# Kernel tuning notes

Hardware: AMD Instinct MI355X
Metric: run time of the kernel (lower is better)

The kernel has to match this reference:

```python
import jax, jax.numpy as jnp
import numpy as np

H = 128  # LSTM hidden size


def lstm_layer(x, Wih, Whh, bih, bhh):
    # x: [B, T, Fin]; Wih: [4H, Fin]; Whh: [4H, H]; biases: [4H]
    xg = jnp.einsum('btf,gf->btg', x, Wih) + bih  # precompute input gates [B,T,4H]
    B = x.shape[0]
    h0 = jnp.zeros((B, H), x.dtype)
    c0 = jnp.zeros((B, H), x.dtype)

    def step(carry, xt):
        h, c = carry
        g = xt + h @ Whh.T + bhh  # [B,4H]
        i, f, gg, o = jnp.split(g, 4, axis=-1)  # torch gate order: i,f,g,o
        i = jax.nn.sigmoid(i)
        f = jax.nn.sigmoid(f)
        gg = jnp.tanh(gg)
        o = jax.nn.sigmoid(o)
        c = f * c + i * gg
        h = o * jnp.tanh(c)
        return (h, c), h

    (hT, cT), hs = jax.lax.scan(step, (h0, c0), jnp.swapaxes(xg, 0, 1))
    return jnp.swapaxes(hs, 0, 1), hT  # all-step outputs [B,T,H], final h [B,H]


def setup_inputs() -> dict:
    key = jax.random.key(0)
    ks = jax.random.split(key, 20)
    B, T, F = 512, 912, 32
    s = 1.0 / np.sqrt(H)  # torch LSTM/Linear init scale
    u = lambda k, shape: jax.random.uniform(k, shape, jnp.float32, -s, s)
    return {
        'x': jax.random.normal(ks[0], (B, T, F), jnp.float32),
        'Wih0': u(ks[1], (4 * H, F)),
        'Whh0': u(ks[2], (4 * H, H)),
        'bih0': u(ks[3], (4 * H,)),
        'bhh0': u(ks[4], (4 * H,)),
        'Wih123': u(ks[5], (3, 4 * H, H)),
        'Whh123': u(ks[6], (3, 4 * H, H)),
        'bih123': u(ks[7], (3, 4 * H)),
        'bhh123': u(ks[8], (3, 4 * H)),
        'Wopt': u(ks[9], (4, H)), 'bopt': u(ks[10], (4,)),
        'Wlot': u(ks[11], (4, H)), 'blot': u(ks[12], (4,)),
        'Wtp': u(ks[13], (4, H)), 'btp': u(ks[14], (4,)),
        'Wsl': u(ks[15], (4, H)), 'bsl': u(ks[16], (4,)),
    }


def reference(x, Wih0, Whh0, bih0, bhh0, Wih123, Whh123, bih123, bhh123,
              Wopt, bopt, Wlot, blot, Wtp, btp, Wsl, bsl):
    out, h0f = lstm_layer(x, Wih0, Whh0, bih0, bhh0)
    finals = [h0f]
    for l in range(3):  # fixed small layer loop
        out, hf = lstm_layer(out, Wih123[l], Whh123[l], bih123[l], bhh123[l])
        finals.append(hf)
    hN = jnp.stack(finals)  # h_n: [4, B, H] (final hidden per layer, as torch returns)
    # heads: Sequential applies softmax/sigmoid once, forward applies it again
    opt = jax.nn.softmax(jax.nn.softmax(hN @ Wopt.T + bopt, axis=-1), axis=-1)
    lot = jax.nn.sigmoid(jax.nn.sigmoid(hN @ Wlot.T + blot))
    tp = jax.nn.sigmoid(jax.nn.sigmoid(hN @ Wtp.T + btp))
    sl = jax.nn.sigmoid(jax.nn.sigmoid(hN @ Wsl.T + bsl))
    return (opt, tp, sl, lot)
```

## Files before the change

kernel.cpp:

```cpp
#include <hip/hip_runtime.h>

#define DEV __device__ __forceinline__

typedef __attribute__((ext_vector_type(8))) short short8;
typedef __attribute__((ext_vector_type(4))) float floatx4;
typedef unsigned long long ull;

static constexpr int B_ = 512, T_ = 912, H_ = 128, F_ = 32;
static constexpr size_t HN_OFF   = 1024;
static constexpr size_t XT_OFF   = HN_OFF + (size_t)4 * 512 * 128 * 2;
static constexpr size_t RING_OFF = XT_OFF + (size_t)T_ * B_ * F_ * 2;
static constexpr size_t RING_BPG = 8 * 32768;

template <int N> struct IC { static constexpr int value = N; };

DEV unsigned short bf16rne(float f) {
    unsigned u = __builtin_bit_cast(unsigned, f);
    u += 0x7FFFu + ((u >> 16) & 1u);
    return (unsigned short)(u >> 16);
}
DEV float bf16tof(unsigned short u) {
    return __builtin_bit_cast(float, ((unsigned)u) << 16);
}
DEV float fastsig(float y) {
    return __builtin_amdgcn_rcpf(1.f + __builtin_amdgcn_exp2f(y));
}
DEV float sigm(float x) { return fastsig(-1.44269504f * x); }
DEV unsigned ald(const unsigned* p) {
    return __hip_atomic_load(p, __ATOMIC_RELAXED, __HIP_MEMORY_SCOPE_AGENT);
}
DEV void ast32(unsigned* p, unsigned v) {
    __hip_atomic_store(p, v, __ATOMIC_RELAXED, __HIP_MEMORY_SCOPE_AGENT);
}
DEV ull ald8(const ull* p) {
    return __hip_atomic_load(p, __ATOMIC_RELAXED, __HIP_MEMORY_SCOPE_AGENT);
}
DEV void ast8(ull* p, ull v) {
    __hip_atomic_store(p, v, __ATOMIC_RELAXED, __HIP_MEMORY_SCOPE_AGENT);
}
DEV void bar_fast() {
    asm volatile("s_waitcnt lgkmcnt(0)\n\ts_barrier" ::: "memory");
}

__global__ __launch_bounds__(256) void xpose(const float* __restrict__ x,
                                             unsigned short* __restrict__ xT) {
    int tid = blockIdx.x * 256 + threadIdx.x;
    if (tid >= B_ * T_ * 4) return;
    int k = tid & 3;
    int r = tid >> 2;
    int b = r / T_;
    int t = r - b * T_;
    const float* p = x + ((size_t)r * 32 + k * 8);
    short8 v;
#pragma unroll
    for (int j = 0; j < 8; j++) v[j] = (short)bf16rne(p[j]);
    *(short8*)(xT + ((size_t)t * 512 + b) * 32 + k * 8) = v;
}

__global__ __launch_bounds__(512, 2) void lstm_scan(
    const float* __restrict__ Wih0, const float* __restrict__ Whh0,
    const float* __restrict__ bih0, const float* __restrict__ bhh0,
    const float* __restrict__ Wih123, const float* __restrict__ Whh123,
    const float* __restrict__ bih123, const float* __restrict__ bhh123,
    char* __restrict__ ws) {
    const int tid  = threadIdx.x;
    const int wv   = tid >> 6;
    const int lane = tid & 63;
    const int col  = lane & 15;
    const int quad = lane >> 4;
    const int layer = blockIdx.x >> 5;
    const int grp   = blockIdx.x & 31;
    const int b0    = grp * 16;

    unsigned* flags = (unsigned*)ws;
    unsigned* cons  = (unsigned*)(ws + 512);
    char* hN8 = ws + HN_OFF;
    const char* xTB = ws + XT_OFF;

    __shared__ unsigned short Ah[16][16][132];
    __shared__ unsigned short Xl[16][16][132];
    char* AhB = (char*)Ah;
    char* XlB = (char*)Xl;

    for (int i = tid; i < 16 * 16 * 132; i += 512) {
        ((unsigned short*)Ah)[i] = 0;
        ((unsigned short*)Xl)[i] = 0;
    }

    short8 wh[4][4];
    short8 wx[4][4];
    float  bias_q[4];
    {
        const float *Wih, *Whh, *bih, *bhh;
        int kin, KX;
        if (layer == 0) { Wih = Wih0; Whh = Whh0; bih = bih0; bhh = bhh0; kin = 32; KX = 1; }
        else {
            Wih = Wih123 + (size_t)(layer - 1) * 512 * 128;
            Whh = Whh123 + (size_t)(layer - 1) * 512 * 128;
            bih = bih123 + (size_t)(layer - 1) * 512;
            bhh = bhh123 + (size_t)(layer - 1) * 512;
            kin = 128; KX = 4;
        }
#pragma unroll
        for (int q = 0; q < 4; q++) {
            const float sc = (q == 2) ? -2.88539008f : -1.44269504f;
            int row = q * 128 + wv * 16 + col;
            bias_q[q] = (bih[row] + bhh[row]) * sc;
#pragma unroll
            for (int kt = 0; kt < 4; kt++) {
                const float* ph = Whh + (size_t)row * 128 + kt * 32 + quad * 8;
                short8 v;
#pragma unroll
                for (int j = 0; j < 8; j++) v[j] = (short)bf16rne(ph[j] * sc);
                wh[q][kt] = v;
            }
#pragma unroll
            for (int kt = 0; kt < 4; kt++) {
                short8 v = {0, 0, 0, 0, 0, 0, 0, 0};
                if (kt < KX) {
                    const float* px = Wih + (size_t)row * kin + kt * 32 + quad * 8;
#pragma unroll
                    for (int j = 0; j < 8; j++) v[j] = (short)bf16rne(px[j] * sc);
                }
                wx[q][kt] = v;
            }
        }
    }

    unsigned* myflag   = &flags[layer * 32 + grp];
    unsigned* prevflag = &flags[(layer > 0 ? layer - 1 : 0) * 32 + grp];
    unsigned* mycons   = &cons[(layer > 0 ? layer - 1 : 0) * 32 + grp];
    unsigned* nextcons = &cons[layer * 32 + grp];
    char* prodRing = ws + RING_OFF + (size_t)(layer * 32 + grp) * RING_BPG;
    char* consRing = ws + RING_OFF + (size_t)((layer > 0 ? layer - 1 : 0) * 32 + grp) * RING_BPG;

    const int ahrd  = col * 264 + quad * 16;
    const int hwr   = (quad * 4) * 264 + (wv * 16 + col) * 2;
    const int exOff = (tid >> 5) * 264 + (tid & 31) * 8;
    const int consOff = (tid >> 5) * 256 + (tid & 31) * 8;
    const int xgOff = (tid >> 6) * 32768 + b0 * 64 + (tid & 63) * 16;
    const int xlw0  = (tid >> 6) * 4224 + ((tid >> 2) & 15) * 264 + (tid & 3) * 16;

    ull    xin[8];
    short8 xv = {0, 0, 0, 0, 0, 0, 0, 0};
    unsigned pf = 0, pc = 0;
    float c4[4] = {0.f, 0.f, 0.f, 0.f};
    floatx4 accx[4];

    __syncthreads();

    if (layer > 0) {
        if (tid == 0) { while (ald(prevflag) < 2u) {} }
        __syncthreads();
#pragma unroll
        for (int j = 0; j < 16; j++) {
            ull d = ald8((const ull*)(consRing + (size_t)j * 4096 + consOff));
            *(ull*)(XlB + exOff + j * 4224) = d;
        }
    } else {
#pragma unroll
        for (int c0 = 0; c0 < 2; c0++) {
            short8 v = *(const short8*)(xTB + (size_t)c0 * 262144 + xgOff);
            *(short8*)(XlB + xlw0 + c0 * 33792) = v;
        }
    }
    __syncthreads();

    {
        short8 ax0[4];
#pragma unroll
        for (int kt = 0; kt < 4; kt++)
            ax0[kt] = *(const short8*)(XlB + ahrd + 0 * 4224 + kt * 64);
#pragma unroll
        for (int q = 0; q < 4; q++) {
            floatx4 a = {bias_q[q], bias_q[q], bias_q[q], bias_q[q]};
            accx[q] = a;
        }
#pragma unroll
        for (int kt = 0; kt < 4; kt++)
#pragma unroll
            for (int q = 0; q < 4; q++)
                accx[q] = __builtin_amdgcn_mfma_f32_16x16x32_bf16(ax0[kt], wx[q][kt], accx[q], 0, 0, 0);
    }

    int c = 0;
    auto step = [&](auto UC) {
        constexpr int u   = UC.value;
        constexpr bool bnd = (u == 0 || u == 8);
        constexpr bool stg = (u == 3 || u == 11);
        constexpr bool ver = (u == 7 || u == 15);
        constexpr int sph = (u < 8) ? 8 : 0;
        const int cc = c + (u >> 3);
        if (bnd) {
            if (tid == 0) {
                if (layer > 0 && cc <= 111) pf = ald(prevflag);
                if (layer < 3 && cc >= 8)   pc = ald(nextcons);
            }
            if (layer < 3 && cc >= 1) {
                char* rb = prodRing + (size_t)((cc - 1) & 7) * 32768 + tid * 8;
#pragma unroll
                for (int p = 0; p < 8; p++) {
                    ull hv = *(const ull*)(AhB + exOff + (sph + p) * 4224);
                    ast8((ull*)(rb + p * 4096), hv);
                }
            }
            if (layer > 0 && cc <= 112) {
                const char* rb2 = consRing + (size_t)((cc + 1) & 7) * 32768 + consOff;
#pragma unroll
                for (int j = 0; j < 8; j++)
                    xin[j] = ald8((const ull*)(rb2 + j * 4096));
            }
            if (layer == 0 && cc <= 112)
                xv = *(const short8*)(xTB + (size_t)(cc + 1) * 262144 + xgOff);
        }
        if (stg) {
            if (layer > 0) {
#pragma unroll
                for (int j = 0; j < 8; j++)
                    *(ull*)(XlB + exOff + (sph + j) * 4224) = xin[j];
            } else {
                *(short8*)(XlB + xlw0 + sph * 4224) = xv;
            }
        }
        short8 ah[4], axn[4];
#pragma unroll
        for (int kt = 0; kt < 4; kt++) {
            ah[kt]  = *(const short8*)(AhB + ahrd + ((u + 15) & 15) * 4224 + kt * 64);
            axn[kt] = *(const short8*)(XlB + ahrd + ((u + 1) & 15) * 4224 + kt * 64);
        }
        floatx4 acc[4];
#pragma unroll
        for (int q = 0; q < 4; q++) acc[q] = accx[q];
#pragma unroll
        for (int kt = 0; kt < 4; kt++)
#pragma unroll
            for (int q = 0; q < 4; q++)
                acc[q] = __builtin_amdgcn_mfma_f32_16x16x32_bf16(ah[kt], wh[q][kt], acc[q], 0, 0, 0);
#pragma unroll
        for (int q = 0; q < 4; q++) {
            floatx4 a = {bias_q[q], bias_q[q], bias_q[q], bias_q[q]};
            accx[q] = a;
        }
#pragma unroll
        for (int r = 0; r < 4; r++) {
            float iv = fastsig(acc[0][r]);
            float fv = fastsig(acc[1][r]);
            float gr = fastsig(acc[2][r]);
            float ov = fastsig(acc[3][r]);
#pragma unroll
            for (int q = 0; q < 4; q++)
                accx[q] = __builtin_amdgcn_mfma_f32_16x16x32_bf16(axn[r], wx[q][r], accx[q], 0, 0, 0);
            float gt = 2.f * gr - 1.f;
            float cv = fv * c4[r] + iv * gt;
            c4[r] = cv;
            float rc = fastsig(-2.88539008f * cv);
            float hv = ov * (2.f * rc - 1.f);
            *(unsigned short*)(AhB + hwr + u * 4224 + r * 264) = bf16rne(hv);
        }
        if (stg) {
            __syncthreads();
            if (tid == 0) {
                if (layer < 3 && cc >= 1) ast32(myflag, (unsigned)cc);
                if (layer > 0) ast32(mycons, (unsigned)(cc + 2));
            }
        } else {
            if (ver && tid == 0) {
                if (layer > 0 && cc <= 111) {
                    unsigned tgt = cc + 3;
                    if (pf < tgt) while (ald(prevflag) < tgt) {}
                }
                if (layer < 3 && cc >= 8) {
                    unsigned tgt = cc - 7;
                    if (pc < tgt) while (ald(nextcons) < tgt) {}
                }
            }
            bar_fast();
        }
    };

    for (c = 0; c < 114; c += 2) {
        step(IC<0>{});  step(IC<1>{});  step(IC<2>{});  step(IC<3>{});
        step(IC<4>{});  step(IC<5>{});  step(IC<6>{});  step(IC<7>{});
        step(IC<8>{});  step(IC<9>{});  step(IC<10>{}); step(IC<11>{});
        step(IC<12>{}); step(IC<13>{}); step(IC<14>{}); step(IC<15>{});
    }

    if (layer < 3) {
        char* rb = prodRing + (size_t)(113 & 7) * 32768 + tid * 8;
#pragma unroll
        for (int p = 0; p < 8; p++) {
            ull hv = *(const ull*)(AhB + exOff + (8 + p) * 4224);
            ast8((ull*)(rb + p * 4096), hv);
        }
    }
    __syncthreads();
    if (tid == 0 && layer < 3) ast32(myflag, 114u);
    {
        ull hv = *(const ull*)(AhB + exOff + 15 * 4224);
        *(ull*)(hN8 + ((size_t)layer * 512 + b0 + (tid >> 5)) * 256 + (tid & 31) * 8) = hv;
    }
}

__global__ __launch_bounds__(256) void heads(
    const unsigned short* __restrict__ hN,
    const float* __restrict__ Wopt, const float* __restrict__ bopt,
    const float* __restrict__ Wlot, const float* __restrict__ blot,
    const float* __restrict__ Wtp,  const float* __restrict__ btp,
    const float* __restrict__ Wsl,  const float* __restrict__ bsl,
    float* __restrict__ out) {
    int tid = blockIdx.x * 256 + threadIdx.x;
    if (tid >= 4 * 4 * 512) return;
    int b  = tid & 511;
    int l  = (tid >> 9) & 3;
    int hd = tid >> 11;
    const float *W, *bb;
    if      (hd == 0) { W = Wopt; bb = bopt; }
    else if (hd == 1) { W = Wtp;  bb = btp;  }
    else if (hd == 2) { W = Wsl;  bb = bsl;  }
    else              { W = Wlot; bb = blot; }
    const unsigned short* h = hN + ((size_t)l * 512 + b) * 128;
    float z0 = bb[0], z1 = bb[1], z2 = bb[2], z3 = bb[3];
    for (int i = 0; i < 128; i++) {
        float hv = bf16tof(h[i]);
        z0 += hv * W[0 * 128 + i];
        z1 += hv * W[1 * 128 + i];
        z2 += hv * W[2 * 128 + i];
        z3 += hv * W[3 * 128 + i];
    }
    float o0, o1, o2, o3;
    if (hd == 0) {
        float m = fmaxf(fmaxf(z0, z1), fmaxf(z2, z3));
        float e0 = __builtin_amdgcn_exp2f((z0 - m) * 1.44269504f);
        float e1 = __builtin_amdgcn_exp2f((z1 - m) * 1.44269504f);
        float e2 = __builtin_amdgcn_exp2f((z2 - m) * 1.44269504f);
        float e3 = __builtin_amdgcn_exp2f((z3 - m) * 1.44269504f);
        float rs = __builtin_amdgcn_rcpf(e0 + e1 + e2 + e3);
        float p0 = e0 * rs, p1 = e1 * rs, p2 = e2 * rs, p3 = e3 * rs;
        float m2 = fmaxf(fmaxf(p0, p1), fmaxf(p2, p3));
        float f0 = __builtin_amdgcn_exp2f((p0 - m2) * 1.44269504f);
        float f1 = __builtin_amdgcn_exp2f((p1 - m2) * 1.44269504f);
        float f2 = __builtin_amdgcn_exp2f((p2 - m2) * 1.44269504f);
        float f3 = __builtin_amdgcn_exp2f((p3 - m2) * 1.44269504f);
        float rs2 = __builtin_amdgcn_rcpf(f0 + f1 + f2 + f3);
        o0 = f0 * rs2; o1 = f1 * rs2; o2 = f2 * rs2; o3 = f3 * rs2;
    } else {
        o0 = sigm(sigm(z0)); o1 = sigm(sigm(z1));
        o2 = sigm(sigm(z2)); o3 = sigm(sigm(z3));
    }
    float* o = out + (size_t)hd * 8192 + ((size_t)l * 512 + b) * 4;
    o[0] = o0; o[1] = o1; o[2] = o2; o[3] = o3;
}

extern "C" void kernel_launch(void* const* d_in, const int* in_sizes, int n_in,
                              void* d_out, int out_size, void* d_ws, size_t ws_size,
                              hipStream_t stream) {
    (void)in_sizes; (void)n_in; (void)out_size; (void)ws_size;
    const float* x      = (const float*)d_in[0];
    const float* Wih0   = (const float*)d_in[1];
    const float* Whh0   = (const float*)d_in[2];
    const float* bih0   = (const float*)d_in[3];
    const float* bhh0   = (const float*)d_in[4];
    const float* Wih123 = (const float*)d_in[5];
    const float* Whh123 = (const float*)d_in[6];
    const float* bih123 = (const float*)d_in[7];
    const float* bhh123 = (const float*)d_in[8];
    const float* Wopt = (const float*)d_in[9];
    const float* bopt = (const float*)d_in[10];
    const float* Wlot = (const float*)d_in[11];
    const float* blot = (const float*)d_in[12];
    const float* Wtp  = (const float*)d_in[13];
    const float* btp  = (const float*)d_in[14];
    const float* Wsl  = (const float*)d_in[15];
    const float* bsl  = (const float*)d_in[16];
    char* ws = (char*)d_ws;

    hipMemsetAsync(ws, 0, 1024, stream);
    xpose<<<(B_ * T_ * 4 + 255) / 256, 256, 0, stream>>>(x, (unsigned short*)(ws + XT_OFF));
    lstm_scan<<<128, 512, 0, stream>>>(Wih0, Whh0, bih0, bhh0,
                                       Wih123, Whh123, bih123, bhh123, ws);
    heads<<<32, 256, 0, stream>>>((const unsigned short*)(ws + HN_OFF),
                                  Wopt, bopt, Wlot, blot, Wtp, btp, Wsl, bsl,
                                  (float*)d_out);
}
```

Baseline: 2.123 ms.

## Load layer inputs directly into MFMA registers and shrink LDS staging ring

Removes the LDS staging buffer for layer inputs. Each step now loads its x operand fragments straight from the global ring, or from the transposed input for layer 0, into double-buffered registers one step ahead. The per-step input projection is fused back into the same step instead of overlapping with the previous step's activations. The h history buffer shrinks from 16 to 8 slots, and producer stores move from chunked bursts to one per step. It also adds s_setprio around the MFMA block. This is meant to cut LDS traffic and footprint, at the cost of putting the x-projection MFMAs on the serial critical path and changing the flag protocol arithmetic.

```diff
diff --git a/kernel.cpp b/kernel.cpp
--- a/kernel.cpp
+++ b/kernel.cpp
@@ -5,6 +5,7 @@
 typedef __attribute__((ext_vector_type(8))) short short8;
 typedef __attribute__((ext_vector_type(4))) float floatx4;
 typedef unsigned long long ull;
+typedef __attribute__((ext_vector_type(2))) unsigned long long ull2;
 
 static constexpr int B_ = 512, T_ = 912, H_ = 128, F_ = 32;
 static constexpr size_t HN_OFF   = 1024;
@@ -71,21 +72,17 @@
     const int layer = blockIdx.x >> 5;
     const int grp   = blockIdx.x & 31;
     const int b0    = grp * 16;
+    const bool lay0 = (layer == 0);
 
     unsigned* flags = (unsigned*)ws;
     unsigned* cons  = (unsigned*)(ws + 512);
     char* hN8 = ws + HN_OFF;
     const char* xTB = ws + XT_OFF;
 
-    __shared__ unsigned short Ah[16][16][132];
-    __shared__ unsigned short Xl[16][16][132];
+    __shared__ unsigned short Ah[8][16][132];
     char* AhB = (char*)Ah;
-    char* XlB = (char*)Xl;
-
-    for (int i = tid; i < 16 * 16 * 132; i += 512) {
-        ((unsigned short*)Ah)[i] = 0;
-        ((unsigned short*)Xl)[i] = 0;
-    }
+
+    for (int i = tid; i < 8 * 16 * 132; i += 512) ((unsigned short*)Ah)[i] = 0;
 
     short8 wh[4][4];
     short8 wx[4][4];
@@ -137,140 +134,136 @@
     const int ahrd  = col * 264 + quad * 16;
     const int hwr   = (quad * 4) * 264 + (wv * 16 + col) * 2;
     const int exOff = (tid >> 5) * 264 + (tid & 31) * 8;
-    const int consOff = (tid >> 5) * 256 + (tid & 31) * 8;
-    const int xgOff = (tid >> 6) * 32768 + b0 * 64 + (tid & 63) * 16;
-    const int xlw0  = (tid >> 6) * 4224 + ((tid >> 2) & 15) * 264 + (tid & 3) * 16;
-
-    ull    xin[8];
-    short8 xv = {0, 0, 0, 0, 0, 0, 0, 0};
+    const int xro   = col * 256 + quad * 16;
+    const int xoffA = (b0 + col) * 64 + quad * 16;
+
+    ull     xnA[8], xnB[8];
+    short8  ax0A = {0,0,0,0,0,0,0,0}, ax0B = ax0A;
     unsigned pf = 0, pc = 0;
     float c4[4] = {0.f, 0.f, 0.f, 0.f};
-    floatx4 accx[4];
 
     __syncthreads();
 
-    if (layer > 0) {
+    if (!lay0) {
         if (tid == 0) { while (ald(prevflag) < 2u) {} }
         __syncthreads();
-#pragma unroll
-        for (int j = 0; j < 16; j++) {
-            ull d = ald8((const ull*)(consRing + (size_t)j * 4096 + consOff));
-            *(ull*)(XlB + exOff + j * 4224) = d;
+        const char* rp = consRing + xro;
+#pragma unroll
+        for (int kt = 0; kt < 4; kt++) {
+            xnA[2 * kt]     = ald8((const ull*)(rp + kt * 64));
+            xnA[2 * kt + 1] = ald8((const ull*)(rp + kt * 64 + 8));
         }
     } else {
-#pragma unroll
-        for (int c0 = 0; c0 < 2; c0++) {
-            short8 v = *(const short8*)(xTB + (size_t)c0 * 262144 + xgOff);
-            *(short8*)(XlB + xlw0 + c0 * 33792) = v;
-        }
-    }
-    __syncthreads();
-
-    {
-        short8 ax0[4];
-#pragma unroll
-        for (int kt = 0; kt < 4; kt++)
-            ax0[kt] = *(const short8*)(XlB + ahrd + 0 * 4224 + kt * 64);
-#pragma unroll
-        for (int q = 0; q < 4; q++) {
-            floatx4 a = {bias_q[q], bias_q[q], bias_q[q], bias_q[q]};
-            accx[q] = a;
-        }
-#pragma unroll
-        for (int kt = 0; kt < 4; kt++)
-#pragma unroll
-            for (int q = 0; q < 4; q++)
-                accx[q] = __builtin_amdgcn_mfma_f32_16x16x32_bf16(ax0[kt], wx[q][kt], accx[q], 0, 0, 0);
+        ax0A = *(const short8*)(xTB + xoffA);
     }
 
     int c = 0;
     auto step = [&](auto UC) {
         constexpr int u   = UC.value;
-        constexpr bool bnd = (u == 0 || u == 8);
-        constexpr bool stg = (u == 3 || u == 11);
-        constexpr bool ver = (u == 7 || u == 15);
-        constexpr int sph = (u < 8) ? 8 : 0;
-        const int cc = c + (u >> 3);
-        if (bnd) {
-            if (tid == 0) {
-                if (layer > 0 && cc <= 111) pf = ald(prevflag);
-                if (layer < 3 && cc >= 8)   pc = ald(nextcons);
-            }
-            if (layer < 3 && cc >= 1) {
-                char* rb = prodRing + (size_t)((cc - 1) & 7) * 32768 + tid * 8;
-#pragma unroll
-                for (int p = 0; p < 8; p++) {
-                    ull hv = *(const ull*)(AhB + exOff + (sph + p) * 4224);
-                    ast8((ull*)(rb + p * 4096), hv);
+        constexpr bool stg = (u == 3);
+        constexpr bool ver = (u == 7);
+        constexpr int eSl = (u + 7) & 7;
+        constexpr int pSl = (u + 1) & 7;
+        constexpr int CUR = u & 1;
+        const int t = c * 8 + u;
+
+        if (u == 0 && tid == 0) {
+            if (layer > 0 && c <= 111) pf = ald(prevflag);
+            if (layer < 3 && c >= 7)   pc = ald(nextcons);
+        }
+
+        short8 ah[4];
+        const char* ab = AhB + eSl * 4224 + ahrd;
+#pragma unroll
+        for (int kt = 0; kt < 4; kt++) ah[kt] = *(const short8*)(ab + kt * 64);
+
+        if (layer < 3 && t > 0) {
+            const int eCh = (u == 0 ? c - 1 : c) & 7;
+            ull hv = *(const ull*)(AhB + eSl * 4224 + exOff);
+            ast8((ull*)(prodRing + (size_t)eCh * 32768 + eSl * 4096 + tid * 8), hv);
+        }
+
+        auto prefetch = [&]() {
+            if (t < 911) {
+                if (!lay0) {
+                    const int pCh = (u == 7 ? c + 1 : c) & 7;
+                    const char* rp = consRing + (size_t)pCh * 32768 + pSl * 4096 + xro;
+#pragma unroll
+                    for (int kt = 0; kt < 4; kt++) {
+                        if (CUR) { xnA[2*kt] = ald8((const ull*)(rp + kt*64));
+                                   xnA[2*kt+1] = ald8((const ull*)(rp + kt*64 + 8)); }
+                        else     { xnB[2*kt] = ald8((const ull*)(rp + kt*64));
+                                   xnB[2*kt+1] = ald8((const ull*)(rp + kt*64 + 8)); }
+                    }
+                } else {
+                    const short8 v = *(const short8*)(xTB + (size_t)(t + 1) * 32768 + xoffA);
+                    if (CUR) ax0A = v; else ax0B = v;
                 }
             }
-            if (layer > 0 && cc <= 112) {
-                const char* rb2 = consRing + (size_t)((cc + 1) & 7) * 32768 + consOff;
-#pragma unroll
-                for (int j = 0; j < 8; j++)
-                    xin[j] = ald8((const ull*)(rb2 + j * 4096));
-            }
-            if (layer == 0 && cc <= 112)
-                xv = *(const short8*)(xTB + (size_t)(cc + 1) * 262144 + xgOff);
-        }
-        if (stg) {
-            if (layer > 0) {
-#pragma unroll
-                for (int j = 0; j < 8; j++)
-                    *(ull*)(XlB + exOff + (sph + j) * 4224) = xin[j];
-            } else {
-                *(short8*)(XlB + xlw0 + sph * 4224) = xv;
-            }
-        }
-        short8 ah[4], axn[4];
-#pragma unroll
-        for (int kt = 0; kt < 4; kt++) {
-            ah[kt]  = *(const short8*)(AhB + ahrd + ((u + 15) & 15) * 4224 + kt * 64);
-            axn[kt] = *(const short8*)(XlB + ahrd + ((u + 1) & 15) * 4224 + kt * 64);
-        }
+        };
+        if constexpr (!stg) prefetch();
+
+        __builtin_amdgcn_s_setprio(1);
         floatx4 acc[4];
 #pragma unroll
-        for (int q = 0; q < 4; q++) acc[q] = accx[q];
+        for (int q = 0; q < 4; q++) {
+            floatx4 a = {bias_q[q], bias_q[q], bias_q[q], bias_q[q]};
+            acc[q] = a;
+        }
+        if (lay0) {
+            const short8 ax = CUR ? ax0B : ax0A;
+#pragma unroll
+            for (int q = 0; q < 4; q++)
+                acc[q] = __builtin_amdgcn_mfma_f32_16x16x32_bf16(ax, wx[q][0], acc[q], 0, 0, 0);
+        } else {
+#pragma unroll
+            for (int kt = 0; kt < 4; kt++) {
+                ull2 p;
+                if (CUR) { p.x = xnB[2*kt]; p.y = xnB[2*kt+1]; }
+                else     { p.x = xnA[2*kt]; p.y = xnA[2*kt+1]; }
+                const short8 ax = __builtin_bit_cast(short8, p);
+#pragma unroll
+                for (int q = 0; q < 4; q++)
+                    acc[q] = __builtin_amdgcn_mfma_f32_16x16x32_bf16(ax, wx[q][kt], acc[q], 0, 0, 0);
+            }
+        }
 #pragma unroll
         for (int kt = 0; kt < 4; kt++)
 #pragma unroll
             for (int q = 0; q < 4; q++)
                 acc[q] = __builtin_amdgcn_mfma_f32_16x16x32_bf16(ah[kt], wh[q][kt], acc[q], 0, 0, 0);
-#pragma unroll
-        for (int q = 0; q < 4; q++) {
-            floatx4 a = {bias_q[q], bias_q[q], bias_q[q], bias_q[q]};
-            accx[q] = a;
-        }
+        __builtin_amdgcn_s_setprio(0);
+
+        char* hb = AhB + (u & 7) * 4224 + hwr;
 #pragma unroll
         for (int r = 0; r < 4; r++) {
             float iv = fastsig(acc[0][r]);
             float fv = fastsig(acc[1][r]);
             float gr = fastsig(acc[2][r]);
             float ov = fastsig(acc[3][r]);
-#pragma unroll
-            for (int q = 0; q < 4; q++)
-                accx[q] = __builtin_amdgcn_mfma_f32_16x16x32_bf16(axn[r], wx[q][r], accx[q], 0, 0, 0);
             float gt = 2.f * gr - 1.f;
             float cv = fv * c4[r] + iv * gt;
             c4[r] = cv;
             float rc = fastsig(-2.88539008f * cv);
             float hv = ov * (2.f * rc - 1.f);
-            *(unsigned short*)(AhB + hwr + u * 4224 + r * 264) = bf16rne(hv);
-        }
-        if (stg) {
+            *(unsigned short*)(hb + r * 264) = bf16rne(hv);
+        }
+
+        if constexpr (stg) {
             __syncthreads();
             if (tid == 0) {
-                if (layer < 3 && cc >= 1) ast32(myflag, (unsigned)cc);
-                if (layer > 0) ast32(mycons, (unsigned)(cc + 2));
-            }
+                if (layer < 3 && c >= 1) ast32(myflag, (unsigned)c);
+                if (layer > 0) ast32(mycons, (unsigned)c);
+            }
+            prefetch();
         } else {
             if (ver && tid == 0) {
-                if (layer > 0 && cc <= 111) {
-                    unsigned tgt = cc + 3;
+                if (layer > 0 && c <= 111) {
+                    unsigned tgt = c + 3;
                     if (pf < tgt) while (ald(prevflag) < tgt) {}
                 }
-                if (layer < 3 && cc >= 8) {
-                    unsigned tgt = cc - 7;
+                if (layer < 3 && c >= 7) {
+                    unsigned tgt = (unsigned)(c - 6);
                     if (pc < tgt) while (ald(nextcons) < tgt) {}
                 }
             }
@@ -278,25 +271,19 @@
         }
     };
 
-    for (c = 0; c < 114; c += 2) {
-        step(IC<0>{});  step(IC<1>{});  step(IC<2>{});  step(IC<3>{});
-        step(IC<4>{});  step(IC<5>{});  step(IC<6>{});  step(IC<7>{});
-        step(IC<8>{});  step(IC<9>{});  step(IC<10>{}); step(IC<11>{});
-        step(IC<12>{}); step(IC<13>{}); step(IC<14>{}); step(IC<15>{});
+    for (c = 0; c < 114; ++c) {
+        step(IC<0>{}); step(IC<1>{}); step(IC<2>{}); step(IC<3>{});
+        step(IC<4>{}); step(IC<5>{}); step(IC<6>{}); step(IC<7>{});
     }
 
     if (layer < 3) {
-        char* rb = prodRing + (size_t)(113 & 7) * 32768 + tid * 8;
-#pragma unroll
-        for (int p = 0; p < 8; p++) {
-            ull hv = *(const ull*)(AhB + exOff + (8 + p) * 4224);
-            ast8((ull*)(rb + p * 4096), hv);
-        }
+        ull hv = *(const ull*)(AhB + 7 * 4224 + exOff);
+        ast8((ull*)(prodRing + (size_t)(113 & 7) * 32768 + 7 * 4096 + tid * 8), hv);
     }
     __syncthreads();
     if (tid == 0 && layer < 3) ast32(myflag, 114u);
     {
-        ull hv = *(const ull*)(AhB + exOff + 15 * 4224);
+        ull hv = *(const ull*)(AhB + 7 * 4224 + exOff);
         *(ull*)(hN8 + ((size_t)layer * 512 + b0 + (tid >> 5)) * 256 + (tid & 31) * 8) = hv;
     }
 }
```

Measured after the change: 3.110 ms. 1.46x slower.

## Spread inter-layer ring stores across steps and prioritize recurrent MFMA chain

Applied to the files above, without the earlier changes.

Instead of writing eight hidden-state slices to the producer ring in one burst at chunk boundaries, each step now stores the previous step's slice right after it is computed. The recurrent h-operand loads are hoisted to the top of the step, and the recurrent MFMA chain runs under raised wave priority via s_setprio. The consumer-progress flag value is also changed to signal the current chunk rather than cc+2. The aim is to smooth global store traffic off the critical path, but the changed flag semantics could alter producer/consumer timing or correctness.

```diff
diff --git a/kernel.cpp b/kernel.cpp
--- a/kernel.cpp
+++ b/kernel.cpp
@@ -190,20 +190,28 @@
         constexpr bool stg = (u == 3 || u == 11);
         constexpr bool ver = (u == 7 || u == 15);
         constexpr int sph = (u < 8) ? 8 : 0;
+        constexpr int hSl = (u + 15) & 15;
         const int cc = c + (u >> 3);
+
+        short8 ah[4];
+        const char* abp = AhB + hSl * 4224 + ahrd;
+#pragma unroll
+        for (int kt = 0; kt < 4; kt++)
+            ah[kt] = *(const short8*)(abp + kt * 64);
+
+        if (layer < 3 && (c > 0 || u > 0)) {
+            constexpr int us  = u & 7;
+            constexpr int eSl = (us + 7) & 7;
+            const int eCh = ((us == 0) ? cc - 1 : cc) & 7;
+            ull hv = *(const ull*)(AhB + hSl * 4224 + exOff);
+            ast8((ull*)(prodRing + (size_t)eCh * 32768 + eSl * 4096 + tid * 8), hv);
+        }
+
         if (bnd) {
             if (tid == 0) {
                 if (layer > 0 && cc <= 111) pf = ald(prevflag);
                 if (layer < 3 && cc >= 8)   pc = ald(nextcons);
             }
-            if (layer < 3 && cc >= 1) {
-                char* rb = prodRing + (size_t)((cc - 1) & 7) * 32768 + tid * 8;
-#pragma unroll
-                for (int p = 0; p < 8; p++) {
-                    ull hv = *(const ull*)(AhB + exOff + (sph + p) * 4224);
-                    ast8((ull*)(rb + p * 4096), hv);
-                }
-            }
             if (layer > 0 && cc <= 112) {
                 const char* rb2 = consRing + (size_t)((cc + 1) & 7) * 32768 + consOff;
 #pragma unroll
@@ -222,20 +230,22 @@
                 *(short8*)(XlB + xlw0 + sph * 4224) = xv;
             }
         }
-        short8 ah[4], axn[4];
-#pragma unroll
-        for (int kt = 0; kt < 4; kt++) {
-            ah[kt]  = *(const short8*)(AhB + ahrd + ((u + 15) & 15) * 4224 + kt * 64);
+        short8 axn[4];
+#pragma unroll
+        for (int kt = 0; kt < 4; kt++)
             axn[kt] = *(const short8*)(XlB + ahrd + ((u + 1) & 15) * 4224 + kt * 64);
-        }
+
         floatx4 acc[4];
 #pragma unroll
         for (int q = 0; q < 4; q++) acc[q] = accx[q];
+        __builtin_amdgcn_s_setprio(1);
 #pragma unroll
         for (int kt = 0; kt < 4; kt++)
 #pragma unroll
             for (int q = 0; q < 4; q++)
                 acc[q] = __builtin_amdgcn_mfma_f32_16x16x32_bf16(ah[kt], wh[q][kt], acc[q], 0, 0, 0);
+        __builtin_amdgcn_s_setprio(0);
+
 #pragma unroll
         for (int q = 0; q < 4; q++) {
             floatx4 a = {bias_q[q], bias_q[q], bias_q[q], bias_q[q]};
@@ -257,11 +267,12 @@
             float hv = ov * (2.f * rc - 1.f);
             *(unsigned short*)(AhB + hwr + u * 4224 + r * 264) = bf16rne(hv);
         }
+
         if (stg) {
             __syncthreads();
             if (tid == 0) {
                 if (layer < 3 && cc >= 1) ast32(myflag, (unsigned)cc);
-                if (layer > 0) ast32(mycons, (unsigned)(cc + 2));
+                if (layer > 0) ast32(mycons, (unsigned)cc);
             }
         } else {
             if (ver && tid == 0) {
@@ -286,17 +297,13 @@
     }
 
     if (layer < 3) {
-        char* rb = prodRing + (size_t)(113 & 7) * 32768 + tid * 8;
-#pragma unroll
-        for (int p = 0; p < 8; p++) {
-            ull hv = *(const ull*)(AhB + exOff + (8 + p) * 4224);
-            ast8((ull*)(rb + p * 4096), hv);
-        }
+        ull hv = *(const ull*)(AhB + 15 * 4224 + exOff);
+        ast8((ull*)(prodRing + (size_t)(113 & 7) * 32768 + 7 * 4096 + tid * 8), hv);
     }
     __syncthreads();
     if (tid == 0 && layer < 3) ast32(myflag, 114u);
     {
-        ull hv = *(const ull*)(AhB + exOff + 15 * 4224);
+        ull hv = *(const ull*)(AhB + 15 * 4224 + exOff);
         *(ull*)(hN8 + ((size_t)layer * 512 + b0 + (tid >> 5)) * 256 + (tid & 31) * 8) = hv;
     }
 }
```

Result: no change. 2.134 ms (+0.5%).
